# Optimization experiments

Hardware: AMD Instinct MI355X
Metric: run time of the kernel (lower is better)

Reference implementation:

```python
import jax, jax.numpy as jnp
import numpy as np

B, D, L, K = 16, 64, 8192, 512


def setup_inputs() -> dict:
    key = jax.random.key(0)
    k1, k2 = jax.random.split(key)
    feature_vectors = jax.random.normal(k1, (B, D, L), dtype=jnp.float32)
    embeddings = jax.random.normal(k2, (D, K), dtype=jnp.float32)  # codebook: latent_dim x num_embeddings
    return {"feature_vectors": feature_vectors, "embeddings": embeddings}


def reference(feature_vectors, embeddings):
    # feature_vectors: (B, D, L); embeddings: (D, K)
    b, d, l = feature_vectors.shape
    k = embeddings.shape[1]
    # tokens: (B*L, D)
    x = jnp.transpose(feature_vectors, (0, 2, 1)).reshape(-1, d)
    x_sq = jnp.sum(x * x, axis=1, keepdims=True)              # (N, 1)
    e_sq = jnp.sum(embeddings * embeddings, axis=0)[None, :]  # (1, K)
    sqdist = x_sq - 2.0 * (x @ embeddings) + e_sq             # (N, K)
    idx_flat = jnp.argmin(sqdist, axis=-1)                    # (N,)
    # gather nearest codebook vectors
    emb_out = jnp.take(embeddings.T, idx_flat, axis=0)        # (N, D)
    closest_embeddings = jnp.transpose(emb_out.reshape(b, l, d), (0, 2, 1))  # (B, D, L)
    closest_indices = idx_flat.reshape(b, l)                  # (B, L)
    return closest_embeddings, closest_indices
```

## Files before the change

kernel.cpp:

```cpp
#include <hip/hip_runtime.h>
#include <float.h>

#define B_ 16
#define D_ 64
#define L_ 8192
#define K_ 512
#define NBLOCKS 512
#define TILES_PER_BLOCK 2
#define EPS 0.0625f


typedef __attribute__((ext_vector_type(8))) _Float16 half8;
typedef __attribute__((ext_vector_type(4))) float    f32x4;

__device__ __forceinline__ unsigned f32_sortable(float x) {
    unsigned u = __float_as_uint(x);
    return u ^ (((int)u >> 31) | 0x80000000u);
}

__global__ __launch_bounds__(512, 2)
void vq_mfma_kernel(const float* __restrict__ X, const float* __restrict__ E,
                    float* __restrict__ out_emb, float* __restrict__ out_idx)
{
    __shared__ __align__(16) short eF[32768];
    __shared__ float esq_s[K_];

    const int tid  = threadIdx.x;
    const int lane = tid & 63;
    const int wave = tid >> 6;
    const int lo4  = lane & 15;
    const int hi4  = lane >> 4;

    {
        _Float16* eH = (_Float16*)eF;
        float s = 0.f;
        int code = tid;
        int blk = code >> 4, c15 = code & 15;
        #pragma unroll 8
        for (int d = 0; d < D_; ++d) {
            float v = E[d * K_ + code];
            float sq = v * v;
            asm volatile("" : "+v"(sq));
            s = s + sq;
            int kh = d >> 5, fl = ((d >> 3) & 3) * 16 + c15, j = d & 7;
            eH[((blk * 2 + kh) * 64 + fl) * 8 + j] = (_Float16)v;
        }
        esq_s[code] = s;
    }
    __syncthreads();

    for (int t = 0; t < TILES_PER_BLOCK; ++t) {
        int tile = blockIdx.x * TILES_PER_BLOCK + t;
        int b  = tile >> 6;
        int l0 = (tile & 63) << 7;
        const int token = wave * 16 + lo4;

        half8 bh0, bh1;
        {
            const float* xb = X + ((size_t)(b * 64 + hi4 * 8)) * L_ + l0 + token;
            #pragma unroll
            for (int j = 0; j < 8; ++j) {
                bh0[j] = (_Float16)xb[(size_t)j * L_];
                bh1[j] = (_Float16)xb[(size_t)(32 + j) * L_];
            }
        }

        float m1 = FLT_MAX, m2 = FLT_MAX;
        int   k1 = 0x7FFFFFFF;
        #pragma unroll 8
        for (int blk = 0; blk < 32; ++blk) {
            half8 ah0 = ((const half8*)eF)[(blk * 2 + 0) * 64 + lane];
            half8 ah1 = ((const half8*)eF)[(blk * 2 + 1) * 64 + lane];
            f32x4 c = {0.f, 0.f, 0.f, 0.f};
            c = __builtin_amdgcn_mfma_f32_16x16x32_f16(ah0, bh0, c, 0, 0, 0);
            c = __builtin_amdgcn_mfma_f32_16x16x32_f16(ah1, bh1, c, 0, 0, 0);
            float4 es4 = *reinterpret_cast<const float4*>(&esq_s[blk * 16 + hi4 * 4]);
            float es[4] = {es4.x, es4.y, es4.z, es4.w};
            #pragma unroll
            for (int r = 0; r < 4; ++r) {
                float sc = fmaf(-2.0f, c[r], es[r]);
                int   cd = blk * 16 + hi4 * 4 + r;
                if (sc < m1)      { m2 = m1; m1 = sc; k1 = cd; }
                else              { m2 = fminf(m2, sc); }
            }
        }

        #pragma unroll
        for (int off = 16; off < 64; off <<= 1) {
            float ov = __shfl_xor(m1, off, 64);
            int   ok = __shfl_xor(k1, off, 64);
            float o2 = __shfl_xor(m2, off, 64);
            float n2 = fminf(fminf(m2, o2), fmaxf(m1, ov));
            if (ov < m1 || (ov == m1 && ok < k1)) { m1 = ov; k1 = ok; }
            m2 = n2;
        }

        unsigned long long bal = __ballot((lane < 16) && (m2 <= m1 + EPS));
        while (bal) {
            int tk = (int)__builtin_ctzll(bal);
            bal &= bal - 1;
            float xs_e;
            {
                int j = lane & 7;
                float r = 0.f;
                #pragma unroll
                for (int m = 0; m < 8; ++m) {
                    float v = X[((size_t)(b * 64 + m * 8 + j)) * L_ + l0 + wave * 16 + tk];
                    float sq = v * v;
                    asm volatile("" : "+v"(sq));
                    r = r + sq;
                }
                r = r + __shfl_xor(r, 1, 64);
                r = r + __shfl_xor(r, 2, 64);
                r = r + __shfl_xor(r, 4, 64);
                xs_e = r;
            }
            float d0 = 0.f, d1 = 0.f, d2 = 0.f, d3 = 0.f;
            float d4 = 0.f, d5 = 0.f, d6 = 0.f, d7 = 0.f;
            const float* Ep = E + 8 * lane;
            #pragma unroll 4
            for (int d = 0; d < 64; ++d) {
                float xv = X[((size_t)(b * 64 + d)) * L_ + l0 + wave * 16 + tk];
                float4 e0 = *reinterpret_cast<const float4*>(Ep + d * K_);
                float4 e1 = *reinterpret_cast<const float4*>(Ep + d * K_ + 4);
                d0 = fmaf(xv, e0.x, d0); d1 = fmaf(xv, e0.y, d1);
                d2 = fmaf(xv, e0.z, d2); d3 = fmaf(xv, e0.w, d3);
                d4 = fmaf(xv, e1.x, d4); d5 = fmaf(xv, e1.y, d5);
                d6 = fmaf(xv, e1.z, d6); d7 = fmaf(xv, e1.w, d7);
            }
            float4 qa = *reinterpret_cast<const float4*>(&esq_s[8 * lane]);
            float4 qb = *reinterpret_cast<const float4*>(&esq_s[8 * lane + 4]);
            float sc[8];
            sc[0] = (xs_e - 2.0f * d0) + qa.x; sc[1] = (xs_e - 2.0f * d1) + qa.y;
            sc[2] = (xs_e - 2.0f * d2) + qa.z; sc[3] = (xs_e - 2.0f * d3) + qa.w;
            sc[4] = (xs_e - 2.0f * d4) + qb.x; sc[5] = (xs_e - 2.0f * d5) + qb.y;
            sc[6] = (xs_e - 2.0f * d6) + qb.z; sc[7] = (xs_e - 2.0f * d7) + qb.w;
            unsigned long long pk = ~0ULL;
            #pragma unroll
            for (int j = 0; j < 8; ++j) {
                unsigned long long p =
                    ((unsigned long long)f32_sortable(sc[j]) << 32) |
                    (unsigned)(8 * lane + j);
                if (p < pk) pk = p;
            }
            #pragma unroll
            for (int off = 1; off < 64; off <<= 1) {
                unsigned long long o = __shfl_xor(pk, off, 64);
                if (o < pk) pk = o;
            }
            int k_ex = (int)(unsigned)(pk & 0xFFFFFFFFULL);
            if (lo4 == tk) k1 = k_ex;
        }

        {
            size_t obase = (size_t)b * 64 * L_ + l0 + token;
            #pragma unroll 4
            for (int dd = 0; dd < 16; ++dd) {
                int d = hi4 * 16 + dd;
                out_emb[obase + (size_t)d * L_] = E[d * K_ + k1];
            }
            if (hi4 == 0)
                out_idx[(size_t)b * L_ + l0 + token] = (float)k1;
        }
    }
}

extern "C" void kernel_launch(void* const* d_in, const int* in_sizes, int n_in,
                              void* d_out, int out_size, void* d_ws, size_t ws_size,
                              hipStream_t stream) {
    const float* X = (const float*)d_in[0];
    const float* E = (const float*)d_in[1];
    float* out     = (float*)d_out;
    float* out_emb = out;
    float* out_idx = out + (size_t)B_ * D_ * L_;
    vq_mfma_kernel<<<NBLOCKS, 512, 0, stream>>>(X, E, out_emb, out_idx);
}
```

Baseline: 71.69 us.

## Stage best indices in LDS for coalesced float4 output writes, fewer blocks

The output gather now goes through shared memory. Each tile's winning code indices are written to LDS, and all threads then emit full-row float4 stores of the gathered embedding values and the index output. This replaces the strided per-token scalar stores. Codebook staging into LDS now uses 16-byte half8 writes instead of scalar half writes. The grid shrinks to 256 blocks of 4 tiles each, which amortizes the codebook setup but halves the number of resident blocks. It also adds a block-wide barrier per tile and reuses the index buffer across tiles without a trailing barrier.

```diff
diff --git a/kernel.cpp b/kernel.cpp
--- a/kernel.cpp
+++ b/kernel.cpp
@@ -5,8 +5,9 @@
 #define D_ 64
 #define L_ 8192
 #define K_ 512
-#define NBLOCKS 512
-#define TILES_PER_BLOCK 2
+#define NBLOCKS 256
+#define TILE_TOK 128
+#define TILES_PER_BLOCK 4
 #define EPS 0.0625f
 
 
@@ -24,6 +25,7 @@
 {
     __shared__ __align__(16) short eF[32768];
     __shared__ float esq_s[K_];
+    __shared__ int   bestk_s[TILE_TOK];
 
     const int tid  = threadIdx.x;
     const int lane = tid & 63;
@@ -32,18 +34,21 @@
     const int hi4  = lane >> 4;
 
     {
-        _Float16* eH = (_Float16*)eF;
-        float s = 0.f;
         int code = tid;
         int blk = code >> 4, c15 = code & 15;
-        #pragma unroll 8
-        for (int d = 0; d < D_; ++d) {
-            float v = E[d * K_ + code];
-            float sq = v * v;
-            asm volatile("" : "+v"(sq));
-            s = s + sq;
-            int kh = d >> 5, fl = ((d >> 3) & 3) * 16 + c15, j = d & 7;
-            eH[((blk * 2 + kh) * 64 + fl) * 8 + j] = (_Float16)v;
+        float s = 0.f;
+        #pragma unroll
+        for (int dd = 0; dd < 8; ++dd) {
+            half8 h8;
+            #pragma unroll
+            for (int j = 0; j < 8; ++j) {
+                float v = E[(dd * 8 + j) * K_ + code];
+                float sq = v * v;
+                asm volatile("" : "+v"(sq));
+                s = s + sq;
+                h8[j] = (_Float16)v;
+            }
+            ((half8*)eF)[(blk * 2 + (dd >> 2)) * 64 + (dd & 3) * 16 + c15] = h8;
         }
         esq_s[code] = s;
     }
@@ -152,16 +157,25 @@
             if (lo4 == tk) k1 = k_ex;
         }
 
+        if (lane < 16) bestk_s[wave * 16 + lo4] = k1;
+        __syncthreads();
         {
-            size_t obase = (size_t)b * 64 * L_ + l0 + token;
-            #pragma unroll 4
-            for (int dd = 0; dd < 16; ++dd) {
-                int d = hi4 * 16 + dd;
-                out_emb[obase + (size_t)d * L_] = E[d * K_ + k1];
+            int d  = tid >> 3;
+            int q8 = tid & 7;
+            #pragma unroll
+            for (int it = 0; it < 4; ++it) {
+                int quad = q8 + it * 8;
+                int i4 = quad * 4;
+                int k0 = bestk_s[i4],     kk1 = bestk_s[i4 + 1];
+                int k2 = bestk_s[i4 + 2], k3  = bestk_s[i4 + 3];
+                float4 v;
+                v.x = E[d * K_ + k0];  v.y = E[d * K_ + kk1];
+                v.z = E[d * K_ + k2];  v.w = E[d * K_ + k3];
+                *reinterpret_cast<float4*>(out_emb + ((size_t)(b * 64 + d)) * L_ + l0 + i4) = v;
             }
-            if (hi4 == 0)
-                out_idx[(size_t)b * L_ + l0 + token] = (float)k1;
         }
+        if (tid < TILE_TOK)
+            out_idx[(size_t)b * L_ + l0 + tid] = (float)bestk_s[tid];
     }
 }
 
```

Result: slower. 82.05 us (+14.4%).
